# Performance work log

Measured on AMD Instinct MI355X. Metric: run time of the kernel, lower is better.

Reference implementation:

```python
import jax, jax.numpy as jnp
import numpy as np

N = 50000
E = 500000
CH = 256
H1, C1 = 4, 64
H2, C2 = 8, 32
CONCAT = H1 * C1 + H2 * C2  # 512


def setup_inputs() -> dict:
    key = jax.random.key(0)
    ks = jax.random.split(key, 16)
    s = 0.05
    x = jax.random.normal(ks[0], (N, CH), dtype=jnp.float32)
    edge_index = jax.random.randint(ks[1], (2, E), 0, N, dtype=jnp.int64)
    return {
        "x": x,
        "edge_index": edge_index,
        "gamma": jnp.ones((CH,), jnp.float32),
        "beta": jnp.zeros((CH,), jnp.float32),
        "W1": jax.random.normal(ks[2], (CH, H1 * C1), jnp.float32) * s,
        "a_src1": jax.random.normal(ks[3], (H1, C1), jnp.float32) * s,
        "a_dst1": jax.random.normal(ks[4], (H1, C1), jnp.float32) * s,
        "b1": jnp.zeros((H1 * C1,), jnp.float32),
        "W2": jax.random.normal(ks[5], (CH, H2 * C2), jnp.float32) * s,
        "a_src2": jax.random.normal(ks[6], (H2, C2), jnp.float32) * s,
        "a_dst2": jax.random.normal(ks[7], (H2, C2), jnp.float32) * s,
        "b2": jnp.zeros((H2 * C2,), jnp.float32),
        "Wu": jax.random.normal(ks[8], (CONCAT, CH), jnp.float32) * s,
        "bu": jnp.zeros((CH,), jnp.float32),
    }


def _layer_norm(x, gamma, beta, eps=1e-5):
    mu = jnp.mean(x, axis=-1, keepdims=True)
    var = jnp.var(x, axis=-1, keepdims=True)
    return (x - mu) * jax.lax.rsqrt(var + eps) * gamma + beta


def _gat_conv(x, src, dst, W, a_src, a_dst, bias, heads, out_ch, n_nodes):
    # x: [N, CH] -> per-head projection h: [N, H, C]
    h = (x @ W).reshape(n_nodes, heads, out_ch)
    alpha_s = jnp.einsum('nhc,hc->nh', h, a_src)  # [N, H]
    alpha_d = jnp.einsum('nhc,hc->nh', h, a_dst)  # [N, H]
    e = jax.nn.leaky_relu(alpha_s[src] + alpha_d[dst], negative_slope=0.2)  # [E, H]
    # segment softmax over incoming edges of each dst node (self-loops guarantee nonempty segments)
    m = jax.ops.segment_max(e, dst, num_segments=n_nodes)
    ex = jnp.exp(e - m[dst])
    denom = jax.ops.segment_sum(ex, dst, num_segments=n_nodes)
    a = ex / (denom[dst] + 1e-16)  # [E, H]
    msg = h[src] * a[:, :, None]  # [E, H, C]
    out = jax.ops.segment_sum(msg, dst, num_segments=n_nodes)  # [N, H, C]
    return out.reshape(n_nodes, heads * out_ch) + bias


def reference(x, edge_index, gamma, beta, W1, a_src1, a_dst1, b1,
              W2, a_src2, a_dst2, b2, Wu, bu):
    n = x.shape[0]
    # add self-loops (PyG GATConv default)
    loop = jnp.arange(n, dtype=edge_index.dtype)
    src = jnp.concatenate([edge_index[0], loop])
    dst = jnp.concatenate([edge_index[1], loop])

    residual = x
    x_norm = _layer_norm(x, gamma, beta)
    out1 = _gat_conv(x_norm, src, dst, W1, a_src1, a_dst1, b1, H1, C1, n)
    out2 = _gat_conv(x_norm, src, dst, W2, a_src2, a_dst2, b2, H2, C2, n)
    x_cat = jax.nn.elu(jnp.concatenate([out1, out2], axis=-1))
    unified = x_cat @ Wu + bu
    return residual + unified
```

## Files before the change

### kernel.cpp

```cpp
#include <hip/hip_runtime.h>
#include <hip/hip_bf16.h>
#include <math.h>

constexpr int CH = 256;
constexpr int CC = 512;
constexpr int AP = 16;

typedef __bf16 bf16x8 __attribute__((ext_vector_type(8)));
typedef float  f32x4  __attribute__((ext_vector_type(4)));
typedef float  f32x2  __attribute__((ext_vector_type(2)));
typedef int    i32x4  __attribute__((ext_vector_type(4)));
typedef __attribute__((address_space(3))) void lds_void;
typedef __attribute__((address_space(1))) void glb_void;

__device__ inline unsigned short f2bf(float f) {
    union { float f; unsigned u; } v; v.f = f;
    unsigned r = v.u + 0x7FFFu + ((v.u >> 16) & 1u);
    return (unsigned short)(r >> 16);
}

__global__ void fused_pre_kernel(const float* __restrict__ x, const float* __restrict__ gamma,
                                 const float* __restrict__ beta,
                                 const float* __restrict__ W1, const float* __restrict__ W2,
                                 const float* __restrict__ Wu,
                                 unsigned short* __restrict__ xnb,
                                 unsigned short* __restrict__ WT1, unsigned short* __restrict__ WTu,
                                 int* __restrict__ deg, int N, int LNB) {
    int b = blockIdx.x;
    int t = threadIdx.x;
    if (b < LNB) {
        int wid = b * 4 + (t >> 6);
        int lane = t & 63;
        if (wid >= N) return;
        const float4 v = *(const float4*)(x + (size_t)wid * CH + lane * 4);
        float s = v.x + v.y + v.z + v.w;
        float sq = v.x * v.x + v.y * v.y + v.z * v.z + v.w * v.w;
        #pragma unroll
        for (int o = 32; o; o >>= 1) { s += __shfl_xor(s, o); sq += __shfl_xor(sq, o); }
        float mu = s * (1.0f / CH);
        float var = sq * (1.0f / CH) - mu * mu;
        float rs = rsqrtf(var + 1e-5f);
        float4 g = *(const float4*)(gamma + lane * 4);
        float4 bb = *(const float4*)(beta + lane * 4);
        unsigned short o0 = f2bf((v.x - mu) * rs * g.x + bb.x);
        unsigned short o1 = f2bf((v.y - mu) * rs * g.y + bb.y);
        unsigned short o2 = f2bf((v.z - mu) * rs * g.z + bb.z);
        unsigned short o3 = f2bf((v.w - mu) * rs * g.w + bb.w);
        uint2 pk;
        pk.x = (unsigned)o0 | ((unsigned)o1 << 16);
        pk.y = (unsigned)o2 | ((unsigned)o3 << 16);
        *(uint2*)(xnb + (size_t)wid * CH + lane * 4) = pk;
    } else if (b < LNB + 512) {
        int idx = (b - LNB) * 256 + t;
        int n = idx >> 8, k = idx & 255;
        float v = (n < 256) ? W1[(size_t)k * 256 + n] : W2[(size_t)k * 256 + (n - 256)];
        WT1[idx] = f2bf(v);
    } else if (b < LNB + 1024) {
        int idx = (b - LNB - 512) * 256 + t;
        int n = idx >> 9, k = idx & 511;
        WTu[idx] = f2bf(Wu[(size_t)k * 256 + n]);
    } else {
        int i = (b - LNB - 1024) * 256 + t;
        if (i < N) deg[i] = 1;
    }
}

template<int K>
__device__ inline void gemm_core_db(const unsigned short* __restrict__ Ab,
                                    const unsigned short* __restrict__ Bt,
                                    unsigned short* As, unsigned short* Bs,
                                    f32x4 acc[4][4], int m0, int n0, int M) {
    const int t = threadIdx.x;
    const int lane = t & 63;
    const int wave = t >> 6;
    const int wr = wave >> 1, wc = wave & 1;
    const int srow = lane >> 3;
    const int scol = (((lane & 7) ^ srow) << 3);
    const int fr = lane & 15;
    const int fkb = (lane >> 4) << 4;

    auto stage = [&](int buf, int k0) {
        #pragma unroll
        for (int c = 0; c < 4; ++c) {
            int chunk = c * 4 + wave;
            int row = chunk * 8 + srow;
            int gra = m0 + row; if (gra >= M) gra = M - 1;
            const unsigned short* ga = Ab + (size_t)gra * K + k0 + scol;
            __builtin_amdgcn_global_load_lds((const glb_void*)ga,
                                             (lds_void*)&As[buf * 8192 + chunk * 512], 16, 0, 0);
            const unsigned short* gb = Bt + (size_t)(n0 + row) * K + k0 + scol;
            __builtin_amdgcn_global_load_lds((const glb_void*)gb,
                                             (lds_void*)&Bs[buf * 8192 + chunk * 512], 16, 0, 0);
        }
    };
    auto compute = [&](int buf) {
        const int bb = buf * 16384;
        #pragma unroll
        for (int ks = 0; ks < 2; ++ks) {
            bf16x8 af[4], bfr[4];
            #pragma unroll
            for (int m = 0; m < 4; ++m) {
                int r = wr * 64 + m * 16 + fr;
                int cb = (ks * 64 + fkb) ^ ((r & 7) << 4);
                af[m] = *(const bf16x8*)((const char*)As + bb + r * 128 + cb);
            }
            #pragma unroll
            for (int n = 0; n < 4; ++n) {
                int r = wc * 64 + n * 16 + fr;
                int cb = (ks * 64 + fkb) ^ ((r & 7) << 4);
                bfr[n] = *(const bf16x8*)((const char*)Bs + bb + r * 128 + cb);
            }
            #pragma unroll
            for (int m = 0; m < 4; ++m)
                #pragma unroll
                for (int n = 0; n < 4; ++n)
                    acc[m][n] = __builtin_amdgcn_mfma_f32_16x16x32_bf16(af[m], bfr[n], acc[m][n], 0, 0, 0);
        }
    };

    stage(0, 0);
    __syncthreads();
    int cur = 0;
    #pragma unroll
    for (int k0 = 64; k0 < K; k0 += 64) {
        stage(cur ^ 1, k0);
        compute(cur);
        __syncthreads();
        cur ^= 1;
    }
    compute(cur);
}

__global__ __launch_bounds__(256) void gemm1_mfma(
    const unsigned short* __restrict__ Ab, const unsigned short* __restrict__ Bt,
    const float* __restrict__ as1, const float* __restrict__ ad1,
    const float* __restrict__ as2, const float* __restrict__ ad2,
    unsigned char* __restrict__ Hq,
    float* __restrict__ alpha_src, float* __restrict__ alpha_dst, int M, int MB,
    const int* __restrict__ dstE, int* __restrict__ deg, int E, int G1B) {
    __shared__ unsigned short As[2 * 128 * 64];
    __shared__ unsigned short Bs[2 * 128 * 64];
    const int s = blockIdx.x;
    if (s >= G1B) {
        int i = (s - G1B) * 256 + threadIdx.x;
        if (i < E) atomicAdd(&deg[dstE[i]], 1);
        return;
    }
    const int xcd = s & 7;
    const int jj = s >> 3;
    const int n_blk = jj & 3;
    const int m_blk = (jj >> 2) * 8 + xcd;
    if (m_blk >= MB) return;
    const int m0 = m_blk * 128, n0 = n_blk * 128;
    const int lane = threadIdx.x & 63;
    const int wave = threadIdx.x >> 6;
    const int wr = wave >> 1, wc = wave & 1;
    f32x4 acc[4][4] = {};
    gemm_core_db<256>(Ab, Bt, As, Bs, acc, m0, n0, M);
    const int fr = lane & 15;
    const int orow = (lane >> 4) * 4;
    #pragma unroll
    for (int m = 0; m < 4; ++m)
        #pragma unroll
        for (int j = 0; j < 4; ++j) {
            int r = m0 + wr * 64 + m * 16 + orow + j;
            if (r < M) {
                #pragma unroll
                for (int n = 0; n < 4; ++n) {
                    int ccol = n0 + wc * 64 + n * 16 + fr;
                    unsigned q = (unsigned)__builtin_amdgcn_cvt_pk_fp8_f32(
                        acc[m][n][j], acc[m][n][j], 0, false) & 0xffu;
                    Hq[(size_t)r * CC + ccol] = (unsigned char)q;
                }
            }
        }
    const int colbase = n0 + wc * 64;
    const bool gat1 = colbase < 256;
    f32x4 svv, dvv;
    int headA;
    if (gat1) {
        headA = colbase >> 6;
        #pragma unroll
        for (int n = 0; n < 4; ++n) { int c = colbase + n * 16 + fr; svv[n] = as1[c]; dvv[n] = ad1[c]; }
    } else {
        headA = 4 + ((colbase - 256) >> 5);
        #pragma unroll
        for (int n = 0; n < 4; ++n) { int c = colbase - 256 + n * 16 + fr; svv[n] = as2[c]; dvv[n] = ad2[c]; }
    }
    __syncthreads();
    float* S = (float*)As + wave * 1024;
    const int g = lane >> 4, kslot = lane & 15;
    const int rown = m0 + wr * 64 + (kslot >> 2) * 16 + g * 4 + (kslot & 3);
    const bool rok = rown < M;
    auto xpose_reduce = [&](f32x4 q0, f32x4 q1, f32x4 q2, f32x4 q3) -> float {
        float* base = S + lane * 16;
        *(f32x4*)(base + 0)  = q0;
        *(f32x4*)(base + 4)  = q1;
        *(f32x4*)(base + 8)  = q2;
        *(f32x4*)(base + 12) = q3;
        const float* rb = S + g * 256 + kslot;
        float sum = 0.f;
        #pragma unroll
        for (int f = 0; f < 16; ++f) sum += rb[f * 16];
        return sum;
    };
    #define PARTF(m, j, W)  (acc[m][0][j]*W[0] + acc[m][1][j]*W[1] + acc[m][2][j]*W[2] + acc[m][3][j]*W[3])
    #define PART01(m, j, W) (acc[m][0][j]*W[0] + acc[m][1][j]*W[1])
    #define PART23(m, j, W) (acc[m][2][j]*W[2] + acc[m][3][j]*W[3])
    #define QUADF(m, W)  (f32x4){PARTF(m,0,W), PARTF(m,1,W), PARTF(m,2,W), PARTF(m,3,W)}
    #define QUAD01(m, W) (f32x4){PART01(m,0,W), PART01(m,1,W), PART01(m,2,W), PART01(m,3,W)}
    #define QUAD23(m, W) (f32x4){PART23(m,0,W), PART23(m,1,W), PART23(m,2,W), PART23(m,3,W)}
    if (gat1) {
        float ts = xpose_reduce(QUADF(0, svv), QUADF(1, svv), QUADF(2, svv), QUADF(3, svv));
        if (rok) alpha_src[(size_t)rown * AP + headA] = ts;
        float td = xpose_reduce(QUADF(0, dvv), QUADF(1, dvv), QUADF(2, dvv), QUADF(3, dvv));
        if (rok) alpha_dst[(size_t)rown * AP + headA] = td;
    } else {
        float s01 = xpose_reduce(QUAD01(0, svv), QUAD01(1, svv), QUAD01(2, svv), QUAD01(3, svv));
        if (rok) alpha_src[(size_t)rown * AP + headA] = s01;
        float s23 = xpose_reduce(QUAD23(0, svv), QUAD23(1, svv), QUAD23(2, svv), QUAD23(3, svv));
        if (rok) alpha_src[(size_t)rown * AP + headA + 1] = s23;
        float d01 = xpose_reduce(QUAD01(0, dvv), QUAD01(1, dvv), QUAD01(2, dvv), QUAD01(3, dvv));
        if (rok) alpha_dst[(size_t)rown * AP + headA] = d01;
        float d23 = xpose_reduce(QUAD23(0, dvv), QUAD23(1, dvv), QUAD23(2, dvv), QUAD23(3, dvv));
        if (rok) alpha_dst[(size_t)rown * AP + headA + 1] = d23;
    }
    #undef PARTF
    #undef PART01
    #undef PART23
    #undef QUADF
    #undef QUAD01
    #undef QUAD23
}

__global__ __launch_bounds__(256) void gemm2_mfma(const unsigned short* __restrict__ Ab,
                                                  const unsigned short* __restrict__ Bt,
                                                  const float* __restrict__ bu,
                                                  const float* __restrict__ xres,
                                                  float* __restrict__ C, int M, int MB) {
    __shared__ unsigned short As[2 * 128 * 64];
    __shared__ unsigned short Bs[2 * 128 * 64];
    const int s = blockIdx.x;
    const int xcd = s & 7;
    const int jj = s >> 3;
    const int n_blk = jj & 1;
    const int m_blk = (jj >> 1) * 8 + xcd;
    if (m_blk >= MB) return;
    const int m0 = m_blk * 128, n0 = n_blk * 128;
    const int lane = threadIdx.x & 63;
    const int wave = threadIdx.x >> 6;
    const int wr = wave >> 1, wc = wave & 1;
    f32x4 acc[4][4] = {};
    gemm_core_db<512>(Ab, Bt, As, Bs, acc, m0, n0, M);
    const int fr = lane & 15;
    const int orow = (lane >> 4) * 4;
    #pragma unroll
    for (int m = 0; m < 4; ++m)
        #pragma unroll
        for (int j = 0; j < 4; ++j) {
            int r = m0 + wr * 64 + m * 16 + orow + j;
            if (r < M) {
                #pragma unroll
                for (int n = 0; n < 4; ++n) {
                    int ccol = n0 + wc * 64 + n * 16 + fr;
                    float xr = __builtin_nontemporal_load(&xres[(size_t)r * CH + ccol]);
                    __builtin_nontemporal_store(acc[m][n][j] + bu[ccol] + xr,
                                                &C[(size_t)r * CH + ccol]);
                }
            }
        }
}

__global__ __launch_bounds__(256) void scan1_kernel(const int* __restrict__ deg, int* __restrict__ pre,
                                                    int* __restrict__ bsum, int n) {
    __shared__ int wsum[4];
    int t = threadIdx.x, lane = t & 63, w = t >> 6;
    int base = blockIdx.x * 1024 + t * 4;
    int v0 = base     < n ? deg[base]     : 0;
    int v1 = base + 1 < n ? deg[base + 1] : 0;
    int v2 = base + 2 < n ? deg[base + 2] : 0;
    int v3 = base + 3 < n ? deg[base + 3] : 0;
    int s = v0 + v1 + v2 + v3;
    int sc = s;
    #pragma unroll
    for (int o = 1; o < 64; o <<= 1) { int xx = __shfl_up(sc, o); if (lane >= o) sc += xx; }
    if (lane == 63) wsum[w] = sc;
    __syncthreads();
    int wo = 0;
    #pragma unroll
    for (int k = 0; k < 4; ++k) if (k < w) wo += wsum[k];
    int p = wo + sc - s;
    if (base     < n) pre[base]     = p; p += v0;
    if (base + 1 < n) pre[base + 1] = p; p += v1;
    if (base + 2 < n) pre[base + 2] = p; p += v2;
    if (base + 3 < n) pre[base + 3] = p;
    if (t == 255) bsum[blockIdx.x] = wo + sc;
}
__global__ void scan2_kernel(int* __restrict__ bsum, int nb) {
    int lane = threadIdx.x;
    int v = lane < nb ? bsum[lane] : 0;
    int sc = v;
    #pragma unroll
    for (int o = 1; o < 64; o <<= 1) { int xx = __shfl_up(sc, o); if (lane >= o) sc += xx; }
    if (lane < nb) bsum[lane] = sc - v;
}
__global__ void scan3_csr_kernel(const int* __restrict__ pre, const int* __restrict__ bsum,
                                 int* __restrict__ offsets, int* __restrict__ cursor,
                                 int* __restrict__ csr, int n, int total) {
    int i = blockIdx.x * 256 + threadIdx.x;
    if (i < n) {
        int off = pre[i] + bsum[i >> 10];
        offsets[i] = off;
        cursor[i] = off + 1;
        csr[off] = i;
    }
    if (i == 0) offsets[n] = total;
}
__global__ void scatter_kernel(const int* __restrict__ src, const int* __restrict__ dst,
                               int* __restrict__ cursor, int* __restrict__ csr, int E) {
    int i = blockIdx.x * blockDim.x + threadIdx.x;
    if (i < E) {
        int pos = atomicAdd(&cursor[dst[i]], 1);
        csr[pos] = src[i];
    }
}

__global__ void aggregate_kernel(const unsigned char* __restrict__ Hq,
                                 const float* __restrict__ alpha_src,
                                 const float* __restrict__ alpha_dst,
                                 const int* __restrict__ offsets,
                                 const int* __restrict__ csr,
                                 const float* __restrict__ b1, const float* __restrict__ b2,
                                 unsigned short* __restrict__ xcb, int N) {
    int n = __builtin_amdgcn_readfirstlane((int)((blockIdx.x * blockDim.x + threadIdx.x) >> 6));
    int lane = threadIdx.x & 63;
    if (n >= N) return;
    int beg = offsets[n], end = offsets[n + 1];
    int c0 = lane * 8;
    int hid = (lane < 32) ? (lane >> 3) : (4 + ((lane - 32) >> 2));
    float adh = alpha_dst[(size_t)n * AP + hid];

    float ssum = 0.f;
    f32x2 A0 = {0.f, 0.f}, A1 = {0.f, 0.f}, A2 = {0.f, 0.f}, A3 = {0.f, 0.f};

    int i = beg;
    for (; i + 4 <= end; i += 4) {
        int ss[4];
        #pragma unroll
        for (int u = 0; u < 4; ++u) ss[u] = csr[i + u];
        float lw[4];
        #pragma unroll
        for (int u = 0; u < 4; ++u) lw[u] = alpha_src[(size_t)ss[u] * AP + hid];
        uint2 hv[4];
        #pragma unroll
        for (int u = 0; u < 4; ++u) hv[u] = *(const uint2*)(Hq + (size_t)ss[u] * CC + c0);
        #pragma unroll
        for (int u = 0; u < 4; ++u) {
            float l = lw[u] + adh;
            l = fmaxf(l, 0.2f * l);
            float wv = __expf(l);
            ssum += wv;
            f32x2 wv2; wv2[0] = wv; wv2[1] = wv;
            A0 += __builtin_amdgcn_cvt_pk_f32_fp8(hv[u].x, false) * wv2;
            A1 += __builtin_amdgcn_cvt_pk_f32_fp8(hv[u].x, true)  * wv2;
            A2 += __builtin_amdgcn_cvt_pk_f32_fp8(hv[u].y, false) * wv2;
            A3 += __builtin_amdgcn_cvt_pk_f32_fp8(hv[u].y, true)  * wv2;
        }
    }
    for (; i < end; ++i) {
        int s0 = csr[i];
        float l = alpha_src[(size_t)s0 * AP + hid] + adh;
        uint2 hv0 = *(const uint2*)(Hq + (size_t)s0 * CC + c0);
        l = fmaxf(l, 0.2f * l);
        float wv = __expf(l);
        ssum += wv;
        f32x2 wv2; wv2[0] = wv; wv2[1] = wv;
        A0 += __builtin_amdgcn_cvt_pk_f32_fp8(hv0.x, false) * wv2;
        A1 += __builtin_amdgcn_cvt_pk_f32_fp8(hv0.x, true)  * wv2;
        A2 += __builtin_amdgcn_cvt_pk_f32_fp8(hv0.y, false) * wv2;
        A3 += __builtin_amdgcn_cvt_pk_f32_fp8(hv0.y, true)  * wv2;
    }

    float inv = 1.0f / (ssum + 1e-16f);
    const float* bb = (c0 < 256) ? (b1 + c0) : (b2 + (c0 - 256));
    float4 bb0 = *(const float4*)(bb), bb1 = *(const float4*)(bb + 4);
    float o[8];
    o[0] = A0[0] * inv + bb0.x; o[1] = A0[1] * inv + bb0.y;
    o[2] = A1[0] * inv + bb0.z; o[3] = A1[1] * inv + bb0.w;
    o[4] = A2[0] * inv + bb1.x; o[5] = A2[1] * inv + bb1.y;
    o[6] = A3[0] * inv + bb1.z; o[7] = A3[1] * inv + bb1.w;
    #pragma unroll
    for (int j = 0; j < 8; ++j) o[j] = o[j] > 0.f ? o[j] : expm1f(o[j]);
    unsigned short u[8];
    #pragma unroll
    for (int j = 0; j < 8; ++j) u[j] = f2bf(o[j]);
    i32x4 pk;
    pk[0] = (int)((unsigned)u[0] | ((unsigned)u[1] << 16));
    pk[1] = (int)((unsigned)u[2] | ((unsigned)u[3] << 16));
    pk[2] = (int)((unsigned)u[4] | ((unsigned)u[5] << 16));
    pk[3] = (int)((unsigned)u[6] | ((unsigned)u[7] << 16));
    __builtin_nontemporal_store(pk, (i32x4*)(xcb + (size_t)n * CC + c0));
}

extern "C" void kernel_launch(void* const* d_in, const int* in_sizes, int n_in,
                              void* d_out, int out_size, void* d_ws, size_t ws_size,
                              hipStream_t stream) {
    const float* x     = (const float*)d_in[0];
    const int*   ei    = (const int*)d_in[1];
    const float* gamma = (const float*)d_in[2];
    const float* beta  = (const float*)d_in[3];
    const float* W1    = (const float*)d_in[4];
    const float* as1   = (const float*)d_in[5];
    const float* ad1   = (const float*)d_in[6];
    const float* b1    = (const float*)d_in[7];
    const float* W2    = (const float*)d_in[8];
    const float* as2   = (const float*)d_in[9];
    const float* ad2   = (const float*)d_in[10];
    const float* b2    = (const float*)d_in[11];
    const float* Wu    = (const float*)d_in[12];
    const float* bu    = (const float*)d_in[13];
    float* out = (float*)d_out;

    const int N = in_sizes[0] / CH;
    const int E = in_sizes[1] / 2;
    const int* src = ei;
    const int* dst = ei + E;

    char* w = (char*)d_ws;
    auto alloc = [&](size_t bytes) { char* p = w; w += (bytes + 255) & ~(size_t)255; return p; };
    unsigned char*  Hq  = (unsigned char*)alloc((size_t)N * CC);
    unsigned short* xnb = (unsigned short*)alloc((size_t)N * CH * 2);
    unsigned short* xcb = (unsigned short*)alloc((size_t)N * CC * 2);
    unsigned short* WT1 = (unsigned short*)alloc(512 * 256 * 2);
    unsigned short* WTu = (unsigned short*)alloc(256 * 512 * 2);
    float* alpha_src = (float*)alloc((size_t)N * AP * 4);
    float* alpha_dst = (float*)alloc((size_t)N * AP * 4);
    int* deg     = (int*)alloc((size_t)N * 4);
    int* pre     = (int*)alloc((size_t)N * 4);
    int* bsum    = (int*)alloc(64 * 4);
    int* offsets = (int*)alloc(((size_t)N + 1) * 4);
    int* cursor  = (int*)alloc((size_t)N * 4);
    int* csr     = (int*)alloc(((size_t)E + N) * 4);

    const int LNB = (N + 3) / 4;
    const int DEGB = (N + 255) / 256;
    fused_pre_kernel<<<LNB + 1024 + DEGB, 256, 0, stream>>>(x, gamma, beta, W1, W2, Wu,
                                                            xnb, WT1, WTu, deg, N, LNB);

    const int MB = (N + 127) / 128;
    const int MB8 = ((MB + 7) / 8) * 8;
    const int G1B = MB8 * 4;
    const int HB = (E + 255) / 256;
    gemm1_mfma<<<G1B + HB, 256, 0, stream>>>(xnb, WT1, as1, ad1, as2, ad2,
                                             Hq, alpha_src, alpha_dst, N, MB,
                                             dst, deg, E, G1B);

    int nb = (N + 1023) / 1024;
    scan1_kernel<<<nb, 256, 0, stream>>>(deg, pre, bsum, N);
    scan2_kernel<<<1, 64, 0, stream>>>(bsum, nb);
    scan3_csr_kernel<<<(N + 255) / 256, 256, 0, stream>>>(pre, bsum, offsets, cursor, csr, N, E + N);
    scatter_kernel<<<(E + 255) / 256, 256, 0, stream>>>(src, dst, cursor, csr, E);

    aggregate_kernel<<<(N + 3) / 4, 256, 0, stream>>>(Hq, alpha_src, alpha_dst, offsets, csr,
                                                      b1, b2, xcb, N);

    gemm2_mfma<<<MB8 * 2, 256, 0, stream>>>(xcb, WTu, bu, x, out, N, MB);
}
```

Measured before the change: 198.7 us.

## Precompute W·a attention projections and compute alpha via separate small GEMM blocks

```diff
diff --git a/kernel.cpp b/kernel.cpp
--- a/kernel.cpp
+++ b/kernel.cpp
@@ -23,9 +23,13 @@
                                  const float* __restrict__ beta,
                                  const float* __restrict__ W1, const float* __restrict__ W2,
                                  const float* __restrict__ Wu,
+                                 const float* __restrict__ as1, const float* __restrict__ ad1,
+                                 const float* __restrict__ as2, const float* __restrict__ ad2,
                                  unsigned short* __restrict__ xnb,
                                  unsigned short* __restrict__ WT1, unsigned short* __restrict__ WTu,
-                                 int* __restrict__ deg, int N, int LNB) {
+                                 unsigned short* __restrict__ Pt,
+                                 const int* __restrict__ dstE, int* __restrict__ deg,
+                                 int N, int E, int LNB) {
     int b = blockIdx.x;
     int t = threadIdx.x;
     if (b < LNB) {
@@ -59,70 +63,80 @@
         int idx = (b - LNB - 512) * 256 + t;
         int n = idx >> 9, k = idx & 511;
         WTu[idx] = f2bf(Wu[(size_t)k * 256 + n]);
+    } else if (b < LNB + 1056) {
+        int n = b - LNB - 1024;
+        int k = t;
+        float a = 0.f;
+        if (n < 4) {
+            for (int c = 0; c < 64; ++c) a += W1[(size_t)k * 256 + n * 64 + c] * as1[n * 64 + c];
+        } else if (n < 12) {
+            for (int c = 0; c < 32; ++c) a += W2[(size_t)k * 256 + (n - 4) * 32 + c] * as2[(n - 4) * 32 + c];
+        } else if (n >= 16 && n < 20) {
+            for (int c = 0; c < 64; ++c) a += W1[(size_t)k * 256 + (n - 16) * 64 + c] * ad1[(n - 16) * 64 + c];
+        } else if (n >= 20 && n < 28) {
+            for (int c = 0; c < 32; ++c) a += W2[(size_t)k * 256 + (n - 20) * 32 + c] * ad2[(n - 20) * 32 + c];
+        }
+        Pt[n * 256 + k] = f2bf(a);
     } else {
-        int i = (b - LNB - 1024) * 256 + t;
-        if (i < N) deg[i] = 1;
+        int i = (b - LNB - 1056) * 256 + t;
+        if (i < E) atomicAdd(&deg[dstE[i]], 1);
     }
 }
 
 template<int K>
-__device__ inline void gemm_core_db(const unsigned short* __restrict__ Ab,
-                                    const unsigned short* __restrict__ Bt,
-                                    unsigned short* As, unsigned short* Bs,
-                                    f32x4 acc[4][4], int m0, int n0, int M) {
+__device__ inline void gemm_core32(const unsigned short* __restrict__ Ab,
+                                   const unsigned short* __restrict__ Bt,
+                                   unsigned short* As, unsigned short* Bs,
+                                   f32x4 acc[4][4], int m0, int n0, int M) {
     const int t = threadIdx.x;
     const int lane = t & 63;
     const int wave = t >> 6;
     const int wr = wave >> 1, wc = wave & 1;
-    const int srow = lane >> 3;
-    const int scol = (((lane & 7) ^ srow) << 3);
+    const int rowc = lane >> 2;
+    const int eslot = lane & 3;
     const int fr = lane & 15;
     const int fkb = (lane >> 4) << 4;
 
     auto stage = [&](int buf, int k0) {
         #pragma unroll
-        for (int c = 0; c < 4; ++c) {
-            int chunk = c * 4 + wave;
-            int row = chunk * 8 + srow;
+        for (int c = 0; c < 2; ++c) {
+            int chunk = wave * 2 + c;
+            int row = chunk * 16 + rowc;
+            int se = ((eslot ^ (row & 3)) << 3);
             int gra = m0 + row; if (gra >= M) gra = M - 1;
-            const unsigned short* ga = Ab + (size_t)gra * K + k0 + scol;
-            __builtin_amdgcn_global_load_lds((const glb_void*)ga,
-                                             (lds_void*)&As[buf * 8192 + chunk * 512], 16, 0, 0);
-            const unsigned short* gb = Bt + (size_t)(n0 + row) * K + k0 + scol;
-            __builtin_amdgcn_global_load_lds((const glb_void*)gb,
-                                             (lds_void*)&Bs[buf * 8192 + chunk * 512], 16, 0, 0);
+            __builtin_amdgcn_global_load_lds((const glb_void*)(Ab + (size_t)gra * K + k0 + se),
+                                             (lds_void*)&As[buf * 4096 + chunk * 512], 16, 0, 0);
+            __builtin_amdgcn_global_load_lds((const glb_void*)(Bt + (size_t)(n0 + row) * K + k0 + se),
+                                             (lds_void*)&Bs[buf * 4096 + chunk * 512], 16, 0, 0);
         }
     };
     auto compute = [&](int buf) {
-        const int bb = buf * 16384;
-        #pragma unroll
-        for (int ks = 0; ks < 2; ++ks) {
-            bf16x8 af[4], bfr[4];
+        const int bb = buf * 8192;
+        bf16x8 af[4], bfr[4];
+        #pragma unroll
+        for (int m = 0; m < 4; ++m) {
+            int r = wr * 64 + m * 16 + fr;
+            int pc = fkb ^ ((r & 3) << 4);
+            af[m] = *(const bf16x8*)((const char*)As + bb + r * 64 + pc);
+        }
+        #pragma unroll
+        for (int n = 0; n < 4; ++n) {
+            int r = wc * 64 + n * 16 + fr;
+            int pc = fkb ^ ((r & 3) << 4);
+            bfr[n] = *(const bf16x8*)((const char*)Bs + bb + r * 64 + pc);
+        }
+        #pragma unroll
+        for (int m = 0; m < 4; ++m)
             #pragma unroll
-            for (int m = 0; m < 4; ++m) {
-                int r = wr * 64 + m * 16 + fr;
-                int cb = (ks * 64 + fkb) ^ ((r & 7) << 4);
-                af[m] = *(const bf16x8*)((const char*)As + bb + r * 128 + cb);
-            }
-            #pragma unroll
-            for (int n = 0; n < 4; ++n) {
-                int r = wc * 64 + n * 16 + fr;
-                int cb = (ks * 64 + fkb) ^ ((r & 7) << 4);
-                bfr[n] = *(const bf16x8*)((const char*)Bs + bb + r * 128 + cb);
-            }
-            #pragma unroll
-            for (int m = 0; m < 4; ++m)
-                #pragma unroll
-                for (int n = 0; n < 4; ++n)
-                    acc[m][n] = __builtin_amdgcn_mfma_f32_16x16x32_bf16(af[m], bfr[n], acc[m][n], 0, 0, 0);
-        }
+            for (int n = 0; n < 4; ++n)
+                acc[m][n] = __builtin_amdgcn_mfma_f32_16x16x32_bf16(af[m], bfr[n], acc[m][n], 0, 0, 0);
     };
 
     stage(0, 0);
     __syncthreads();
     int cur = 0;
     #pragma unroll
-    for (int k0 = 64; k0 < K; k0 += 64) {
+    for (int k0 = 32; k0 < K; k0 += 32) {
         stage(cur ^ 1, k0);
         compute(cur);
         __syncthreads();
@@ -133,104 +147,115 @@
 
 __global__ __launch_bounds__(256) void gemm1_mfma(
     const unsigned short* __restrict__ Ab, const unsigned short* __restrict__ Bt,
-    const float* __restrict__ as1, const float* __restrict__ ad1,
-    const float* __restrict__ as2, const float* __restrict__ ad2,
+    const unsigned short* __restrict__ Pt,
     unsigned char* __restrict__ Hq,
-    float* __restrict__ alpha_src, float* __restrict__ alpha_dst, int M, int MB,
-    const int* __restrict__ dstE, int* __restrict__ deg, int E, int G1B) {
-    __shared__ unsigned short As[2 * 128 * 64];
-    __shared__ unsigned short Bs[2 * 128 * 64];
+    float* __restrict__ alpha_src, float* __restrict__ alpha_dst, int M, int MB, int G1B) {
+    __shared__ unsigned short As[8192];
+    __shared__ unsigned short Bs[8192];
     const int s = blockIdx.x;
-    if (s >= G1B) {
-        int i = (s - G1B) * 256 + threadIdx.x;
-        if (i < E) atomicAdd(&deg[dstE[i]], 1);
-        return;
-    }
-    const int xcd = s & 7;
-    const int jj = s >> 3;
-    const int n_blk = jj & 3;
-    const int m_blk = (jj >> 2) * 8 + xcd;
-    if (m_blk >= MB) return;
-    const int m0 = m_blk * 128, n0 = n_blk * 128;
     const int lane = threadIdx.x & 63;
     const int wave = threadIdx.x >> 6;
-    const int wr = wave >> 1, wc = wave & 1;
-    f32x4 acc[4][4] = {};
-    gemm_core_db<256>(Ab, Bt, As, Bs, acc, m0, n0, M);
     const int fr = lane & 15;
+    const int fkb = (lane >> 4) << 4;
     const int orow = (lane >> 4) * 4;
-    #pragma unroll
-    for (int m = 0; m < 4; ++m)
-        #pragma unroll
-        for (int j = 0; j < 4; ++j) {
-            int r = m0 + wr * 64 + m * 16 + orow + j;
-            if (r < M) {
-                #pragma unroll
-                for (int n = 0; n < 4; ++n) {
-                    int ccol = n0 + wc * 64 + n * 16 + fr;
-                    unsigned q = (unsigned)__builtin_amdgcn_cvt_pk_fp8_f32(
-                        acc[m][n][j], acc[m][n][j], 0, false) & 0xffu;
-                    Hq[(size_t)r * CC + ccol] = (unsigned char)q;
+
+    if (s < G1B) {
+        const int xcd = s & 7;
+        const int jj = s >> 3;
+        const int n_blk = jj & 3;
+        const int m_blk = (jj >> 2) * 8 + xcd;
+        if (m_blk >= MB) return;
+        const int m0 = m_blk * 128, n0 = n_blk * 128;
+        const int wr = wave >> 1, wc = wave & 1;
+        f32x4 acc[4][4] = {};
+        gemm_core32<256>(Ab, Bt, As, Bs, acc, m0, n0, M);
+        #pragma unroll
+        for (int m = 0; m < 4; ++m)
+            #pragma unroll
+            for (int j = 0; j < 4; ++j) {
+                int r = m0 + wr * 64 + m * 16 + orow + j;
+                if (r < M) {
+                    #pragma unroll
+                    for (int n = 0; n < 4; ++n) {
+                        int ccol = n0 + wc * 64 + n * 16 + fr;
+                        unsigned q = (unsigned)__builtin_amdgcn_cvt_pk_fp8_f32(
+                            acc[m][n][j], acc[m][n][j], 0, false) & 0xffu;
+                        Hq[(size_t)r * CC + ccol] = (unsigned char)q;
+                    }
                 }
             }
-        }
-    const int colbase = n0 + wc * 64;
-    const bool gat1 = colbase < 256;
-    f32x4 svv, dvv;
-    int headA;
-    if (gat1) {
-        headA = colbase >> 6;
-        #pragma unroll
-        for (int n = 0; n < 4; ++n) { int c = colbase + n * 16 + fr; svv[n] = as1[c]; dvv[n] = ad1[c]; }
-    } else {
-        headA = 4 + ((colbase - 256) >> 5);
-        #pragma unroll
-        for (int n = 0; n < 4; ++n) { int c = colbase - 256 + n * 16 + fr; svv[n] = as2[c]; dvv[n] = ad2[c]; }
-    }
+        return;
+    }
+    const int m_blk = s - G1B;
+    if (m_blk >= MB) return;
+    const int m0 = m_blk * 128;
+    {
+        int rr_in = lane >> 5;
+        int e32 = lane & 31;
+        #pragma unroll
+        for (int c = 0; c < 4; ++c) {
+            int chunk = wave * 4 + c;
+            int rr = chunk * 2 + rr_in;
+            const unsigned short* g = Pt + rr * 256 + ((e32 ^ (rr & 7)) << 3);
+            __builtin_amdgcn_global_load_lds((const glb_void*)g,
+                                             (lds_void*)&Bs[chunk * 512], 16, 0, 0);
+        }
+    }
+    const int rowc = lane >> 2, eslot = lane & 3;
+    auto stageA = [&](int buf, int k0) {
+        #pragma unroll
+        for (int c = 0; c < 2; ++c) {
+            int chunk = wave * 2 + c;
+            int row = chunk * 16 + rowc;
+            int gra = m0 + row; if (gra >= M) gra = M - 1;
+            const unsigned short* g = Ab + (size_t)gra * 256 + k0 + ((eslot ^ (row & 3)) << 3);
+            __builtin_amdgcn_global_load_lds((const glb_void*)g,
+                                             (lds_void*)&As[buf * 4096 + chunk * 512], 16, 0, 0);
+        }
+    };
+    f32x4 a2[2][2] = {};
+    auto computeA = [&](int buf, int k0) {
+        const int bb = buf * 8192;
+        bf16x8 af[2], bf_[2];
+        #pragma unroll
+        for (int m = 0; m < 2; ++m) {
+            int r = wave * 32 + m * 16 + fr;
+            int pc = fkb ^ ((r & 3) << 4);
+            af[m] = *(const bf16x8*)((const char*)As + bb + r * 64 + pc);
+        }
+        #pragma unroll
+        for (int n = 0; n < 2; ++n) {
+            int rb = n * 16 + fr;
+            int pcb = (k0 * 2 + fkb) ^ ((rb & 7) << 4);
+            bf_[n] = *(const bf16x8*)((const char*)Bs + rb * 512 + pcb);
+        }
+        #pragma unroll
+        for (int m = 0; m < 2; ++m)
+            #pragma unroll
+            for (int n = 0; n < 2; ++n)
+                a2[m][n] = __builtin_amdgcn_mfma_f32_16x16x32_bf16(af[m], bf_[n], a2[m][n], 0, 0, 0);
+    };
+    stageA(0, 0);
     __syncthreads();
-    float* S = (float*)As + wave * 1024;
-    const int g = lane >> 4, kslot = lane & 15;
-    const int rown = m0 + wr * 64 + (kslot >> 2) * 16 + g * 4 + (kslot & 3);
-    const bool rok = rown < M;
-    auto xpose_reduce = [&](f32x4 q0, f32x4 q1, f32x4 q2, f32x4 q3) -> float {
-        float* base = S + lane * 16;
-        *(f32x4*)(base + 0)  = q0;
-        *(f32x4*)(base + 4)  = q1;
-        *(f32x4*)(base + 8)  = q2;
-        *(f32x4*)(base + 12) = q3;
-        const float* rb = S + g * 256 + kslot;
-        float sum = 0.f;
-        #pragma unroll
-        for (int f = 0; f < 16; ++f) sum += rb[f * 16];
-        return sum;
-    };
-    #define PARTF(m, j, W)  (acc[m][0][j]*W[0] + acc[m][1][j]*W[1] + acc[m][2][j]*W[2] + acc[m][3][j]*W[3])
-    #define PART01(m, j, W) (acc[m][0][j]*W[0] + acc[m][1][j]*W[1])
-    #define PART23(m, j, W) (acc[m][2][j]*W[2] + acc[m][3][j]*W[3])
-    #define QUADF(m, W)  (f32x4){PARTF(m,0,W), PARTF(m,1,W), PARTF(m,2,W), PARTF(m,3,W)}
-    #define QUAD01(m, W) (f32x4){PART01(m,0,W), PART01(m,1,W), PART01(m,2,W), PART01(m,3,W)}
-    #define QUAD23(m, W) (f32x4){PART23(m,0,W), PART23(m,1,W), PART23(m,2,W), PART23(m,3,W)}
-    if (gat1) {
-        float ts = xpose_reduce(QUADF(0, svv), QUADF(1, svv), QUADF(2, svv), QUADF(3, svv));
-        if (rok) alpha_src[(size_t)rown * AP + headA] = ts;
-        float td = xpose_reduce(QUADF(0, dvv), QUADF(1, dvv), QUADF(2, dvv), QUADF(3, dvv));
-        if (rok) alpha_dst[(size_t)rown * AP + headA] = td;
-    } else {
-        float s01 = xpose_reduce(QUAD01(0, svv), QUAD01(1, svv), QUAD01(2, svv), QUAD01(3, svv));
-        if (rok) alpha_src[(size_t)rown * AP + headA] = s01;
-        float s23 = xpose_reduce(QUAD23(0, svv), QUAD23(1, svv), QUAD23(2, svv), QUAD23(3, svv));
-        if (rok) alpha_src[(size_t)rown * AP + headA + 1] = s23;
-        float d01 = xpose_reduce(QUAD01(0, dvv), QUAD01(1, dvv), QUAD01(2, dvv), QUAD01(3, dvv));
-        if (rok) alpha_dst[(size_t)rown * AP + headA] = d01;
-        float d23 = xpose_reduce(QUAD23(0, dvv), QUAD23(1, dvv), QUAD23(2, dvv), QUAD23(3, dvv));
-        if (rok) alpha_dst[(size_t)rown * AP + headA + 1] = d23;
-    }
-    #undef PARTF
-    #undef PART01
-    #undef PART23
-    #undef QUADF
-    #undef QUAD01
-    #undef QUAD23
+    int cur = 0;
+    #pragma unroll
+    for (int k0 = 32; k0 < 256; k0 += 32) {
+        stageA(cur ^ 1, k0);
+        computeA(cur, k0 - 32);
+        __syncthreads();
+        cur ^= 1;
+    }
+    computeA(cur, 224);
+    #pragma unroll
+    for (int m = 0; m < 2; ++m)
+        #pragma unroll
+        for (int j = 0; j < 4; ++j) {
+            int r = m0 + wave * 32 + m * 16 + orow + j;
+            if (fr < 12 && r < M) {
+                alpha_src[(size_t)r * AP + fr] = a2[m][0][j];
+                alpha_dst[(size_t)r * AP + fr] = a2[m][1][j];
+            }
+        }
 }
 
 __global__ __launch_bounds__(256) void gemm2_mfma(const unsigned short* __restrict__ Ab,
@@ -238,8 +263,8 @@
                                                   const float* __restrict__ bu,
                                                   const float* __restrict__ xres,
                                                   float* __restrict__ C, int M, int MB) {
-    __shared__ unsigned short As[2 * 128 * 64];
-    __shared__ unsigned short Bs[2 * 128 * 64];
+    __shared__ unsigned short As[8192];
+    __shared__ unsigned short Bs[8192];
     const int s = blockIdx.x;
     const int xcd = s & 7;
     const int jj = s >> 3;
@@ -251,7 +276,7 @@
     const int wave = threadIdx.x >> 6;
     const int wr = wave >> 1, wc = wave & 1;
     f32x4 acc[4][4] = {};
-    gemm_core_db<512>(Ab, Bt, As, Bs, acc, m0, n0, M);
+    gemm_core32<512>(Ab, Bt, As, Bs, acc, m0, n0, M);
     const int fr = lane & 15;
     const int orow = (lane >> 4) * 4;
     #pragma unroll
@@ -276,10 +301,10 @@
     __shared__ int wsum[4];
     int t = threadIdx.x, lane = t & 63, w = t >> 6;
     int base = blockIdx.x * 1024 + t * 4;
-    int v0 = base     < n ? deg[base]     : 0;
-    int v1 = base + 1 < n ? deg[base + 1] : 0;
-    int v2 = base + 2 < n ? deg[base + 2] : 0;
-    int v3 = base + 3 < n ? deg[base + 3] : 0;
+    int v0 = base     < n ? deg[base]     + 1 : 0;
+    int v1 = base + 1 < n ? deg[base + 1] + 1 : 0;
+    int v2 = base + 2 < n ? deg[base + 2] + 1 : 0;
+    int v3 = base + 3 < n ? deg[base + 3] + 1 : 0;
     int s = v0 + v1 + v2 + v3;
     int sc = s;
     #pragma unroll
@@ -433,6 +458,7 @@
     unsigned short* xcb = (unsigned short*)alloc((size_t)N * CC * 2);
     unsigned short* WT1 = (unsigned short*)alloc(512 * 256 * 2);
     unsigned short* WTu = (unsigned short*)alloc(256 * 512 * 2);
+    unsigned short* Pt  = (unsigned short*)alloc(32 * 256 * 2);
     float* alpha_src = (float*)alloc((size_t)N * AP * 4);
     float* alpha_dst = (float*)alloc((size_t)N * AP * 4);
     int* deg     = (int*)alloc((size_t)N * 4);
@@ -442,18 +468,18 @@
     int* cursor  = (int*)alloc((size_t)N * 4);
     int* csr     = (int*)alloc(((size_t)E + N) * 4);
 
+    hipMemsetAsync(deg, 0, (size_t)N * 4, stream);
+
     const int LNB = (N + 3) / 4;
-    const int DEGB = (N + 255) / 256;
-    fused_pre_kernel<<<LNB + 1024 + DEGB, 256, 0, stream>>>(x, gamma, beta, W1, W2, Wu,
-                                                            xnb, WT1, WTu, deg, N, LNB);
+    const int HB = (E + 255) / 256;
+    fused_pre_kernel<<<LNB + 1056 + HB, 256, 0, stream>>>(
+        x, gamma, beta, W1, W2, Wu, as1, ad1, as2, ad2,
+        xnb, WT1, WTu, Pt, dst, deg, N, E, LNB);
 
     const int MB = (N + 127) / 128;
     const int MB8 = ((MB + 7) / 8) * 8;
     const int G1B = MB8 * 4;
-    const int HB = (E + 255) / 256;
-    gemm1_mfma<<<G1B + HB, 256, 0, stream>>>(xnb, WT1, as1, ad1, as2, ad2,
-                                             Hq, alpha_src, alpha_dst, N, MB,
-                                             dst, deg, E, G1B);
+    gemm1_mfma<<<G1B + MB, 256, 0, stream>>>(xnb, WT1, Pt, Hq, alpha_src, alpha_dst, N, MB, G1B);
 
     int nb = (N + 1023) / 1024;
     scan1_kernel<<<nb, 256, 0, stream>>>(deg, pre, bsum, N);
```

Result: slower. 204.4 us (+2.9%).
